# Optimization experiments

Hardware: AMD Instinct MI355X
Metric: run time of the kernel (lower is better)

The kernel has to match this reference:

```python
import jax, jax.numpy as jnp
import numpy as np

N = 50000
E = 800000
D = 128  # input_dim = hidden_dim = output_dim
N_LAYERS = 3


def _graph_conv(x, src, dst, edge_weight, w_rel, b_rel, w_root):
    # PyG GraphConv (aggr='add'):
    #   out = lin_rel( sum_{j in N(i)} edge_weight_ij * x_j ) + lin_root(x_i)
    msg = x[src] * edge_weight[:, None]                      # [E, D_in]
    agg = jax.ops.segment_sum(msg, dst, num_segments=x.shape[0])  # [N, D_in]
    return agg @ w_rel + b_rel + x @ w_root                  # [N, D_out]


def setup_inputs() -> dict:
    key = jax.random.key(0)
    ks = jax.random.split(key, 4 + 3 * N_LAYERS)
    x = jax.random.normal(ks[0], (N, D), dtype=jnp.float32)
    edge_index = jax.random.randint(ks[1], (2, E), 0, N, dtype=jnp.int32)
    edge_attr = jax.random.uniform(ks[2], (E,), dtype=jnp.float32)
    scale = 1.0 / np.sqrt(D)
    inp = {"x": x, "edge_index": edge_index, "edge_attr": edge_attr}
    for l in range(N_LAYERS):
        inp[f"w_rel{l}"] = jax.random.normal(ks[3 + 3 * l], (D, D), dtype=jnp.float32) * scale
        inp[f"b_rel{l}"] = jnp.zeros((D,), dtype=jnp.float32)
        inp[f"w_root{l}"] = jax.random.normal(ks[4 + 3 * l], (D, D), dtype=jnp.float32) * scale
    return inp


def reference(x, edge_index, edge_attr,
              w_rel0, b_rel0, w_root0,
              w_rel1, b_rel1, w_root1,
              w_rel2, b_rel2, w_root2):
    src, dst = edge_index[0], edge_index[1]
    params = [(w_rel0, b_rel0, w_root0), (w_rel1, b_rel1, w_root1), (w_rel2, b_rel2, w_root2)]
    h = x
    for w_rel, b_rel, w_root in params[:-1]:
        h = _graph_conv(h, src, dst, edge_attr, w_rel, b_rel, w_root)
        h = jax.nn.relu(h)  # dropout p=0.0 -> identity
    w_rel, b_rel, w_root = params[-1]
    return _graph_conv(h, src, dst, edge_attr, w_rel, b_rel, w_root)
```

## Files before the change

kernel.cpp:

```cpp
#include <hip/hip_runtime.h>
#include <hip/hip_bf16.h>
#include <hip/hip_fp16.h>

#define N_NODES 50000
#define N_EDGES 800000
#define DIM 128

#define NBUCK 391
#define BCAP  2816
#define CHUNK 2048

#define CVT_BLOCKS 25000

#define LDSROW 136

typedef float floatx4 __attribute__((ext_vector_type(4)));
typedef float floatx2 __attribute__((ext_vector_type(2)));
typedef short shortx8 __attribute__((ext_vector_type(8)));

__device__ __forceinline__ unsigned short f2bf(float f) {
    union { float f; unsigned int u; } c; c.f = f;
    unsigned int u = c.u;
    unsigned int r = (u + 0x7FFFu + ((u >> 16) & 1u)) >> 16;
    return (unsigned short)r;
}
__device__ __forceinline__ floatx2 bf2x2(unsigned int p) {
    union { unsigned int u; float f; } lo, hi;
    lo.u = p << 16; hi.u = p & 0xFFFF0000u;
    return (floatx2){lo.f, hi.f};
}

__global__ __launch_bounds__(256)
void prep_kernel(const float* __restrict__ x, unsigned short* __restrict__ X,
                 const float* __restrict__ wr0, const float* __restrict__ wt0,
                 const float* __restrict__ wr1, const float* __restrict__ wt1,
                 const float* __restrict__ wr2, const float* __restrict__ wt2,
                 unsigned short* __restrict__ Wp, int* __restrict__ bcursor) {
    int b = blockIdx.x;
    if (b < CVT_BLOCKS) {
        int i = b * 256 + threadIdx.x;
        X[i] = f2bf(x[i]);
    } else if (b == CVT_BLOCKS) {
        for (int i = threadIdx.x; i < NBUCK; i += 256) bcursor[i] = 0;
    } else {
        int id = (b - CVT_BLOCKS - 1) * 256 + threadIdx.x;
        int layer = id >> 15;
        int rem = id & 32767;
        int j  = rem & 7;
        int L  = (rem >> 3) & 63;
        int ct = (rem >> 9) & 7;
        int t  = rem >> 12;
        int k = t * 32 + (L >> 4) * 8 + j;
        int c = ct * 16 + (L & 15);
        const float* wr = (layer == 0) ? wr0 : (layer == 1) ? wr1 : wr2;
        const float* wt = (layer == 0) ? wt0 : (layer == 1) ? wt1 : wt2;
        float v = (k < 128) ? wr[k * 128 + c] : wt[(k - 128) * 128 + c];
        Wp[id] = f2bf(v);
    }
}

__global__ __launch_bounds__(1024)
void partition_kernel(const int* __restrict__ src, const int* __restrict__ dst,
                      const float* __restrict__ ew,
                      int* __restrict__ bcursor, int2* __restrict__ bstage, int e) {
    __shared__ int2 stage[CHUNK];
    __shared__ int cnt[NBUCK];
    __shared__ int lbase[NBUCK];
    __shared__ int gbase[NBUCK];
    __shared__ int wsum[16];
    const int tid = threadIdx.x;
    const int e0 = blockIdx.x * CHUNK;
    const int ecnt = min(CHUNK, e - e0);

    for (int i = tid; i < NBUCK; i += 1024) cnt[i] = 0;
    __syncthreads();
    for (int i = tid; i < ecnt; i += 1024)
        atomicAdd(&cnt[dst[e0 + i] >> 7], 1);
    __syncthreads();

    {
        int v = (tid < NBUCK) ? cnt[tid] : 0;
        int lane = tid & 63, wid = tid >> 6;
        int acc = v;
#pragma unroll
        for (int off = 1; off < 64; off <<= 1) {
            int t = __shfl_up(acc, off, 64);
            if (lane >= off) acc += t;
        }
        if (lane == 63) wsum[wid] = acc;
        __syncthreads();
        int wpref = 0;
        for (int w = 0; w < wid; ++w) wpref += wsum[w];
        int excl = wpref + acc - v;
        if (tid < NBUCK) {
            lbase[tid] = excl;
            gbase[tid] = atomicAdd(&bcursor[tid], v);
            cnt[tid] = 0;
        }
    }
    __syncthreads();

    for (int i = tid; i < ecnt; i += 1024) {
        int d = dst[e0 + i];
        int s = src[e0 + i];
        unsigned int hw = (unsigned int)__half_as_ushort(__float2half(ew[e0 + i]));
        int b = d >> 7;
        int pos = atomicAdd(&cnt[b], 1);
        stage[lbase[b] + pos] = make_int2((int)((hw << 16) | (unsigned int)s), d);
    }
    __syncthreads();

    for (int j = tid; j < ecnt; j += 1024) {
        int2 p = stage[j];
        int b = p.y >> 7;
        int gidx = b * BCAP + gbase[b] + (j - lbase[b]);
        bstage[gidx] = p;
    }
}

__global__ __launch_bounds__(512)
void bucket_fill_kernel(const int2* __restrict__ bstage, const int* __restrict__ bcursor,
                        int* __restrict__ row_start, unsigned int* __restrict__ perm4, int n) {
    __shared__ int cnt128[128];
    __shared__ int curs[128];
    __shared__ int wsum[8];
    __shared__ int sbase, scnt;
    const int tid = threadIdx.x;
    const int b = blockIdx.x;
    const int node0 = b << 7;
    const int lane = tid & 63, wid = tid >> 6;

    {
        int v = (tid < NBUCK) ? bcursor[tid] : 0;
        int acc = v;
#pragma unroll
        for (int off = 1; off < 64; off <<= 1) {
            int t = __shfl_up(acc, off, 64);
            if (lane >= off) acc += t;
        }
        if (lane == 63) wsum[wid] = acc;
        __syncthreads();
        int wpref = 0;
        for (int w = 0; w < wid; ++w) wpref += wsum[w];
        int excl = wpref + acc - v;
        if (tid == b) { sbase = excl; scnt = v; }
    }
    __syncthreads();
    const int cntb = scnt;
    const int base = sbase;
    const int2* sp = bstage + (size_t)b * BCAP;

    if (tid < 128) cnt128[tid] = 0;
    __syncthreads();
    for (int i = tid; i < cntb; i += 512)
        atomicAdd(&cnt128[sp[i].y & 127], 1);
    __syncthreads();

    int v = (tid < 128) ? cnt128[tid] : 0;
    int acc = v;
#pragma unroll
    for (int off = 1; off < 64; off <<= 1) {
        int t = __shfl_up(acc, off, 64);
        if (lane >= off) acc += t;
    }
    if (lane == 63) wsum[wid] = acc;
    __syncthreads();
    int wpref = 0;
    for (int w = 0; w < wid; ++w) wpref += wsum[w];
    int excl = wpref + acc - v;
    if (tid < 128) {
        int node = node0 + tid;
        if (node <= n) row_start[node] = base + excl;
        curs[tid] = excl;
    }
    __syncthreads();

    for (int i = tid; i < cntb; i += 512) {
        int2 p = sp[i];
        int pos = atomicAdd(&curs[p.y & 127], 1);
        perm4[base + pos] = (unsigned int)p.x;
    }
}

__global__ __launch_bounds__(256, 8)
void fused_layer(const unsigned short* __restrict__ h, const int* __restrict__ row_start,
                 const unsigned int* __restrict__ perm4, const unsigned short* __restrict__ Wp,
                 const float* __restrict__ bias, float* __restrict__ outF,
                 unsigned short* __restrict__ outB, int relu) {
    __shared__ unsigned short Gs[16 * LDSROW];
    const int tid  = threadIdx.x;
    const int lane = tid & 63;
    const int wid  = tid >> 6;
    const int g  = lane >> 4;
    const int sl = lane & 15;
    const int rowT = blockIdx.x * 16;
    const int nodeBase = rowT + wid * 4;

    int rs = 0;
    if (lane < 5) rs = row_start[nodeBase + lane];
    const int beg = __shfl(rs, g, 64);
    const int end = __shfl(rs, g + 1, 64);

    floatx2 ac[4];
#pragma unroll
    for (int k = 0; k < 4; ++k) ac[k] = (floatx2){0.f, 0.f};
    const unsigned short* hp = h + sl * 8;
    for (int t = beg; t < end; t += 4) {
        unsigned int p0 = perm4[t];
        unsigned int p1 = (t + 1 < end) ? perm4[t + 1] : 0;
        unsigned int p2 = (t + 2 < end) ? perm4[t + 2] : 0;
        unsigned int p3 = (t + 3 < end) ? perm4[t + 3] : 0;
        uint4 v0 = *(const uint4*)(hp + (size_t)(p0 & 0xFFFF) * DIM);
        uint4 v1 = *(const uint4*)(hp + (size_t)(p1 & 0xFFFF) * DIM);
        uint4 v2 = *(const uint4*)(hp + (size_t)(p2 & 0xFFFF) * DIM);
        uint4 v3 = *(const uint4*)(hp + (size_t)(p3 & 0xFFFF) * DIM);
        float w0 = __half2float(__ushort_as_half((unsigned short)(p0 >> 16)));
        float w1 = __half2float(__ushort_as_half((unsigned short)(p1 >> 16)));
        float w2 = __half2float(__ushort_as_half((unsigned short)(p2 >> 16)));
        float w3 = __half2float(__ushort_as_half((unsigned short)(p3 >> 16)));
        floatx2 W0 = (floatx2){w0, w0}, W1 = (floatx2){w1, w1};
        floatx2 W2 = (floatx2){w2, w2}, W3 = (floatx2){w3, w3};
        ac[0] += W0 * bf2x2(v0.x); ac[1] += W0 * bf2x2(v0.y);
        ac[2] += W0 * bf2x2(v0.z); ac[3] += W0 * bf2x2(v0.w);
        ac[0] += W1 * bf2x2(v1.x); ac[1] += W1 * bf2x2(v1.y);
        ac[2] += W1 * bf2x2(v1.z); ac[3] += W1 * bf2x2(v1.w);
        ac[0] += W2 * bf2x2(v2.x); ac[1] += W2 * bf2x2(v2.y);
        ac[2] += W2 * bf2x2(v2.z); ac[3] += W2 * bf2x2(v2.w);
        ac[0] += W3 * bf2x2(v3.x); ac[1] += W3 * bf2x2(v3.y);
        ac[2] += W3 * bf2x2(v3.z); ac[3] += W3 * bf2x2(v3.w);
    }
    {
        uint4 r;
        r.x = (unsigned int)f2bf(ac[0].x) | ((unsigned int)f2bf(ac[0].y) << 16);
        r.y = (unsigned int)f2bf(ac[1].x) | ((unsigned int)f2bf(ac[1].y) << 16);
        r.z = (unsigned int)f2bf(ac[2].x) | ((unsigned int)f2bf(ac[2].y) << 16);
        r.w = (unsigned int)f2bf(ac[3].x) | ((unsigned int)f2bf(ac[3].y) << 16);
        *(uint4*)(&Gs[(wid * 4 + g) * LDSROW + sl * 8]) = r;
    }
    __syncthreads();

    floatx4 acc2[2];
#pragma unroll
    for (int ct = 0; ct < 2; ++ct) acc2[ct] = (floatx4){0.f, 0.f, 0.f, 0.f};

    const int rr = rowT + sl;
    const int ko = g * 8;
#pragma unroll
    for (int t = 0; t < 8; ++t) {
        shortx8 a;
        if (t < 4)
            a = *(const shortx8*)(&Gs[sl * LDSROW + t * 32 + ko]);
        else
            a = *(const shortx8*)(h + (size_t)rr * DIM + (t - 4) * 32 + ko);
        const unsigned short* wp = Wp + (size_t)t * 4096 + (wid * 2) * 512 + lane * 8;
#pragma unroll
        for (int ct = 0; ct < 2; ++ct) {
            shortx8 b = *(const shortx8*)(wp + ct * 512);
            acc2[ct] = __builtin_amdgcn_mfma_f32_16x16x32_bf16(a, b, acc2[ct], 0, 0, 0);
        }
    }

#pragma unroll
    for (int ct = 0; ct < 2; ++ct) {
        int col = wid * 32 + ct * 16 + sl;
        float bv = bias[col];
#pragma unroll
        for (int i = 0; i < 4; ++i) {
            int row = rowT + g * 4 + i;
            float v = acc2[ct][i] + bv;
            if (relu) v = fmaxf(v, 0.f);
            if (outF) outF[(size_t)row * DIM + col] = v;
            else      outB[(size_t)row * DIM + col] = f2bf(v);
        }
    }
}

extern "C" void kernel_launch(void* const* d_in, const int* in_sizes, int n_in,
                              void* d_out, int out_size, void* d_ws, size_t ws_size,
                              hipStream_t stream) {
    const int N = N_NODES, E = N_EDGES;

    const float* x   = (const float*)d_in[0];
    const int*   ei  = (const int*)d_in[1];
    const float* ea  = (const float*)d_in[2];
    const float* wr0 = (const float*)d_in[3];
    const float* br0 = (const float*)d_in[4];
    const float* wt0 = (const float*)d_in[5];
    const float* wr1 = (const float*)d_in[6];
    const float* br1 = (const float*)d_in[7];
    const float* wt1 = (const float*)d_in[8];
    const float* wr2 = (const float*)d_in[9];
    const float* br2 = (const float*)d_in[10];
    const float* wt2 = (const float*)d_in[11];
    const int* srcI = ei;
    const int* dstI = ei + E;
    float* out = (float*)d_out;

    int2* bstage = (int2*)d_ws;
    unsigned short* X  = (unsigned short*)(bstage + (size_t)NBUCK * BCAP);
    unsigned short* H1 = X + (size_t)N * DIM;
    unsigned short* H2 = H1 + (size_t)N * DIM;
    unsigned short* Wp = H2 + (size_t)N * DIM;
    unsigned int* perm4 = (unsigned int*)(Wp + 3 * 32768);
    int* bcursor = (int*)(perm4 + E);
    int* rowst   = bcursor + NBUCK;

    prep_kernel<<<CVT_BLOCKS + 1 + 384, 256, 0, stream>>>(x, X, wr0, wt0, wr1, wt1, wr2, wt2, Wp, bcursor);
    partition_kernel<<<(E + CHUNK - 1) / CHUNK, 1024, 0, stream>>>(srcI, dstI, ea, bcursor, bstage, E);
    bucket_fill_kernel<<<NBUCK, 512, 0, stream>>>(bstage, bcursor, rowst, perm4, N);

    const int fusedGrid = N / 16;

    fused_layer<<<fusedGrid, 256, 0, stream>>>(X,  rowst, perm4, Wp,         br0, nullptr, H1, 1);
    fused_layer<<<fusedGrid, 256, 0, stream>>>(H1, rowst, perm4, Wp + 32768, br1, nullptr, H2, 1);
    fused_layer<<<fusedGrid, 256, 0, stream>>>(H2, rowst, perm4, Wp + 65536, br2, out, nullptr, 0);
}
```

Measured before the change: 236.1 us.

## Software-pipeline edge gathers and overlap root GEMM before block barrier

The neighbor gather loop is double-buffered: the next group of four perm entries and h rows is loaded before the current group is accumulated, which hides global load latency. The root-term MFMAs, which read h directly, now run before __syncthreads so that independent work overlaps the wait for other waves' aggregation. Launch bounds drop occupancy from 8 to 6 to give room for the extra registers, which reduces the number of waves available to hide latency.

```diff
diff --git a/kernel.cpp b/kernel.cpp
--- a/kernel.cpp
+++ b/kernel.cpp
@@ -182,7 +182,14 @@
     }
 }
 
-__global__ __launch_bounds__(256, 8)
+#define ACCQ(p, v) do { \
+    float w_ = __half2float(__ushort_as_half((unsigned short)((p) >> 16))); \
+    floatx2 W_ = (floatx2){w_, w_}; \
+    ac[0] += W_ * bf2x2((v).x); ac[1] += W_ * bf2x2((v).y); \
+    ac[2] += W_ * bf2x2((v).z); ac[3] += W_ * bf2x2((v).w); \
+} while (0)
+
+__global__ __launch_bounds__(256, 6)
 void fused_layer(const unsigned short* __restrict__ h, const int* __restrict__ row_start,
                  const unsigned int* __restrict__ perm4, const unsigned short* __restrict__ Wp,
                  const float* __restrict__ bias, float* __restrict__ outF,
@@ -205,30 +212,35 @@
 #pragma unroll
     for (int k = 0; k < 4; ++k) ac[k] = (floatx2){0.f, 0.f};
     const unsigned short* hp = h + sl * 8;
-    for (int t = beg; t < end; t += 4) {
-        unsigned int p0 = perm4[t];
-        unsigned int p1 = (t + 1 < end) ? perm4[t + 1] : 0;
-        unsigned int p2 = (t + 2 < end) ? perm4[t + 2] : 0;
-        unsigned int p3 = (t + 3 < end) ? perm4[t + 3] : 0;
-        uint4 v0 = *(const uint4*)(hp + (size_t)(p0 & 0xFFFF) * DIM);
-        uint4 v1 = *(const uint4*)(hp + (size_t)(p1 & 0xFFFF) * DIM);
-        uint4 v2 = *(const uint4*)(hp + (size_t)(p2 & 0xFFFF) * DIM);
-        uint4 v3 = *(const uint4*)(hp + (size_t)(p3 & 0xFFFF) * DIM);
-        float w0 = __half2float(__ushort_as_half((unsigned short)(p0 >> 16)));
-        float w1 = __half2float(__ushort_as_half((unsigned short)(p1 >> 16)));
-        float w2 = __half2float(__ushort_as_half((unsigned short)(p2 >> 16)));
-        float w3 = __half2float(__ushort_as_half((unsigned short)(p3 >> 16)));
-        floatx2 W0 = (floatx2){w0, w0}, W1 = (floatx2){w1, w1};
-        floatx2 W2 = (floatx2){w2, w2}, W3 = (floatx2){w3, w3};
-        ac[0] += W0 * bf2x2(v0.x); ac[1] += W0 * bf2x2(v0.y);
-        ac[2] += W0 * bf2x2(v0.z); ac[3] += W0 * bf2x2(v0.w);
-        ac[0] += W1 * bf2x2(v1.x); ac[1] += W1 * bf2x2(v1.y);
-        ac[2] += W1 * bf2x2(v1.z); ac[3] += W1 * bf2x2(v1.w);
-        ac[0] += W2 * bf2x2(v2.x); ac[1] += W2 * bf2x2(v2.y);
-        ac[2] += W2 * bf2x2(v2.z); ac[3] += W2 * bf2x2(v2.w);
-        ac[0] += W3 * bf2x2(v3.x); ac[1] += W3 * bf2x2(v3.y);
-        ac[2] += W3 * bf2x2(v3.z); ac[3] += W3 * bf2x2(v3.w);
-    }
+    const bool any = beg < end;
+    unsigned int pA0 = 0, pA1 = 0, pA2 = 0, pA3 = 0;
+    uint4 vA0 = {}, vA1 = {}, vA2 = {}, vA3 = {};
+    int t = beg;
+    if (any) {
+        pA0 = perm4[t];
+        pA1 = (t + 1 < end) ? perm4[t + 1] : 0u;
+        pA2 = (t + 2 < end) ? perm4[t + 2] : 0u;
+        pA3 = (t + 3 < end) ? perm4[t + 3] : 0u;
+        vA0 = *(const uint4*)(hp + (size_t)(pA0 & 0xFFFFu) * DIM);
+        vA1 = *(const uint4*)(hp + (size_t)(pA1 & 0xFFFFu) * DIM);
+        vA2 = *(const uint4*)(hp + (size_t)(pA2 & 0xFFFFu) * DIM);
+        vA3 = *(const uint4*)(hp + (size_t)(pA3 & 0xFFFFu) * DIM);
+    }
+    for (; t + 4 < end; t += 4) {
+        unsigned int pB0 = perm4[t + 4];
+        unsigned int pB1 = (t + 5 < end) ? perm4[t + 5] : 0u;
+        unsigned int pB2 = (t + 6 < end) ? perm4[t + 6] : 0u;
+        unsigned int pB3 = (t + 7 < end) ? perm4[t + 7] : 0u;
+        uint4 vB0 = *(const uint4*)(hp + (size_t)(pB0 & 0xFFFFu) * DIM);
+        uint4 vB1 = *(const uint4*)(hp + (size_t)(pB1 & 0xFFFFu) * DIM);
+        uint4 vB2 = *(const uint4*)(hp + (size_t)(pB2 & 0xFFFFu) * DIM);
+        uint4 vB3 = *(const uint4*)(hp + (size_t)(pB3 & 0xFFFFu) * DIM);
+        ACCQ(pA0, vA0); ACCQ(pA1, vA1); ACCQ(pA2, vA2); ACCQ(pA3, vA3);
+        pA0 = pB0; pA1 = pB1; pA2 = pB2; pA3 = pB3;
+        vA0 = vB0; vA1 = vB1; vA2 = vB2; vA3 = vB3;
+    }
+    if (any) { ACCQ(pA0, vA0); ACCQ(pA1, vA1); ACCQ(pA2, vA2); ACCQ(pA3, vA3); }
+
     {
         uint4 r;
         r.x = (unsigned int)f2bf(ac[0].x) | ((unsigned int)f2bf(ac[0].y) << 16);
@@ -237,22 +249,29 @@
         r.w = (unsigned int)f2bf(ac[3].x) | ((unsigned int)f2bf(ac[3].y) << 16);
         *(uint4*)(&Gs[(wid * 4 + g) * LDSROW + sl * 8]) = r;
     }
-    __syncthreads();
 
     floatx4 acc2[2];
 #pragma unroll
     for (int ct = 0; ct < 2; ++ct) acc2[ct] = (floatx4){0.f, 0.f, 0.f, 0.f};
-
     const int rr = rowT + sl;
     const int ko = g * 8;
 #pragma unroll
-    for (int t = 0; t < 8; ++t) {
-        shortx8 a;
-        if (t < 4)
-            a = *(const shortx8*)(&Gs[sl * LDSROW + t * 32 + ko]);
-        else
-            a = *(const shortx8*)(h + (size_t)rr * DIM + (t - 4) * 32 + ko);
-        const unsigned short* wp = Wp + (size_t)t * 4096 + (wid * 2) * 512 + lane * 8;
+    for (int t2 = 4; t2 < 8; ++t2) {
+        shortx8 a = *(const shortx8*)(h + (size_t)rr * DIM + (t2 - 4) * 32 + ko);
+        const unsigned short* wp = Wp + (size_t)t2 * 4096 + (wid * 2) * 512 + lane * 8;
+#pragma unroll
+        for (int ct = 0; ct < 2; ++ct) {
+            shortx8 b = *(const shortx8*)(wp + ct * 512);
+            acc2[ct] = __builtin_amdgcn_mfma_f32_16x16x32_bf16(a, b, acc2[ct], 0, 0, 0);
+        }
+    }
+
+    __syncthreads();
+
+#pragma unroll
+    for (int t2 = 0; t2 < 4; ++t2) {
+        shortx8 a = *(const shortx8*)(&Gs[sl * LDSROW + t2 * 32 + ko]);
+        const unsigned short* wp = Wp + (size_t)t2 * 4096 + (wid * 2) * 512 + lane * 8;
 #pragma unroll
         for (int ct = 0; ct < 2; ++ct) {
             shortx8 b = *(const shortx8*)(wp + ct * 512);
```

Measured after the change: 231.9 us. Within noise of the previous version (-1.7%).
